# Kernel tuning notes

Measured on AMD Instinct MI355X. Metric: run time of the kernel, lower is better.

Reference implementation:

```python
import jax, jax.numpy as jnp
import numpy as np

B, T, D_MODEL = 2, 2048, 2048
NUM_HEADS, NUM_KV_HEADS, HEAD_DIM = 16, 16, 128
NUM_Q_HEADS = 2 * NUM_HEADS  # diff-v2 doubles the query heads


def _rope_freqs(seqlen, dim_half, base=10000.0):
    inv = 1.0 / (base ** (np.arange(0, dim_half, dtype=np.float32) / dim_half))
    t = np.arange(seqlen, dtype=np.float32)
    ang = np.outer(t, inv)  # [T, dim_half]
    return jnp.asarray(np.cos(ang)), jnp.asarray(np.sin(ang))


def apply_rotary_interleaved(x, cos, sin):
    # x: [B, T, H, D]; cos/sin: [T, D//2]; pairs are adjacent (interleaved=True)
    x1, x2 = x[..., 0::2], x[..., 1::2]
    c = cos[None, :, None, :]
    s = sin[None, :, None, :]
    o1 = x1 * c - x2 * s
    o2 = x1 * s + x2 * c
    return jnp.stack([o1, o2], axis=-1).reshape(x.shape)


def setup_inputs() -> dict:
    key = jax.random.key(0)
    ks = jax.random.split(key, 6)
    x = jax.random.normal(ks[0], (B, T, D_MODEL), dtype=jnp.float32)
    cos, sin = _rope_freqs(T, HEAD_DIM // 2)
    sc = 1.0 / np.sqrt(D_MODEL)
    Wq = jax.random.normal(ks[1], (D_MODEL, NUM_Q_HEADS * HEAD_DIM), dtype=jnp.float32) * sc
    Wk = jax.random.normal(ks[2], (D_MODEL, NUM_KV_HEADS * HEAD_DIM), dtype=jnp.float32) * sc
    Wv = jax.random.normal(ks[3], (D_MODEL, NUM_KV_HEADS * HEAD_DIM), dtype=jnp.float32) * sc
    Wo = jax.random.normal(ks[4], (NUM_HEADS * HEAD_DIM, D_MODEL), dtype=jnp.float32) * sc
    Wlam = jax.random.normal(ks[5], (D_MODEL, NUM_HEADS), dtype=jnp.float32) * sc
    return {"x": x, "cos": cos, "sin": sin, "Wq": Wq, "Wk": Wk, "Wv": Wv, "Wo": Wo, "Wlam": Wlam}


def reference(x, cos, sin, Wq, Wk, Wv, Wo, Wlam):
    b, t, _ = x.shape
    q = (x @ Wq).reshape(b, t, NUM_Q_HEADS, HEAD_DIM)
    k = (x @ Wk).reshape(b, t, NUM_KV_HEADS, HEAD_DIM)
    v = (x @ Wv).reshape(b, t, NUM_KV_HEADS, HEAD_DIM)
    q = apply_rotary_interleaved(q, cos, sin)
    k = apply_rotary_interleaved(k, cos, sin)
    # GQA: repeat kv heads to match the doubled query heads
    rep = NUM_Q_HEADS // NUM_KV_HEADS
    k = jnp.repeat(k, rep, axis=2)
    v = jnp.repeat(v, rep, axis=2)
    scale = 1.0 / np.sqrt(HEAD_DIM)
    scores = jnp.einsum('bthd,bshd->bhts', q, k) * scale  # [B, 2H, T, T]
    causal = jnp.tril(jnp.ones((t, t), dtype=bool))
    scores = jnp.where(causal[None, None], scores, jnp.finfo(scores.dtype).min)
    p = jax.nn.softmax(scores, axis=-1)
    attn = jnp.einsum('bhts,bshd->bthd', p, v)  # [B, T, 2H, D]
    lam = jax.nn.sigmoid(x @ Wlam)  # [B, T, H]
    attn1, attn2 = attn[:, :, 0::2], attn[:, :, 1::2]
    out = attn1 - lam[..., None] * attn2  # [B, T, H, D]
    return out.reshape(b, t, NUM_HEADS * HEAD_DIM) @ Wo
```

## Files before the change

### kernel.cpp

```cpp
#include <hip/hip_runtime.h>

#define T_SEQ 2048
#define BATCH 2
#define DMODEL 2048
#define NQH 32
#define NKVH 16
#define HD 128

typedef _Float16 f16;
typedef _Float16 f16x8 __attribute__((ext_vector_type(8)));
typedef _Float16 f16x4 __attribute__((ext_vector_type(4)));
typedef _Float16 f16x2 __attribute__((ext_vector_type(2)));
typedef float f32x4 __attribute__((ext_vector_type(4)));

typedef const __attribute__((address_space(1))) void* gptr_t;
typedef __attribute__((address_space(3))) void* sptr_t;
#define GLDS16(g, l) __builtin_amdgcn_global_load_lds((gptr_t)(g), (sptr_t)(l), 16, 0, 0)

__global__ __launch_bounds__(256) void k_transpose_all(const float* __restrict__ Wq,
                                                       const float* __restrict__ Wk,
                                                       const float* __restrict__ Wv,
                                                       const float* __restrict__ Wo,
                                                       f16* __restrict__ WqkvT,
                                                       f16* __restrict__ WoT) {
  __shared__ float tile[32][33];
  const int z = blockIdx.z;
  const float* W;
  f16* WT;
  int N;
  if (z == 0)      { W = Wq; WT = WqkvT;                          N = 4096; }
  else if (z == 1) { W = Wk; WT = WqkvT + (size_t)4096 * 2048;    N = 2048; }
  else if (z == 2) { W = Wv; WT = WqkvT + (size_t)6144 * 2048;    N = 2048; }
  else             { W = Wo; WT = WoT;                            N = 2048; }
  const int K = 2048;
  int n0 = blockIdx.x * 32;
  if (n0 >= N) return;
  int k0 = blockIdx.y * 32;
  int tx = threadIdx.x & 31;
  int ty0 = threadIdx.x >> 5;
  #pragma unroll
  for (int i = 0; i < 4; ++i) {
    int ty = ty0 + i * 8;
    tile[ty][tx] = W[(size_t)(k0 + ty) * N + n0 + tx];
  }
  __syncthreads();
  #pragma unroll
  for (int i = 0; i < 4; ++i) {
    int ty = ty0 + i * 8;
    WT[(size_t)(n0 + ty) * K + k0 + tx] = (f16)tile[tx][ty];
  }
}

template<int BM, int BN, int WM, int WN, int OM>
__global__ __launch_bounds__(512, 1) void k_gemm3(const f16* __restrict__ A,
                                                  const f16* __restrict__ BT,
                                                  void* __restrict__ C0,
                                                  f16* __restrict__ Kh,
                                                  f16* __restrict__ VTg,
                                                  const float* __restrict__ cosb,
                                                  const float* __restrict__ sinb,
                                                  int M, int N, int K) {
  constexpr int MR = BM / WM / 16;
  constexpr int MR2 = MR / 2;
  constexpr int NR = BN / WN / 16;
  constexpr int ACH = BM / 64;
  constexpr int BCH = BN / 64;
  __shared__ alignas(16) f16 Al[2][BM * 64];
  __shared__ alignas(16) f16 Bl[2][BN * 64];
  const int tid = threadIdx.x;
  const int lane = tid & 63;
  const int w = tid >> 6;
  const int wr = w / WN, wc = w % WN;
  const int lr = lane & 15, lg = lane >> 4;
  const int nbx = N / BN;
  const int cpx = gridDim.x >> 3;
  const int wg = (blockIdx.x & 7) * cpx + (blockIdx.x >> 3);
  const int m0 = (wg / nbx) * BM, n0 = (wg % nbx) * BN;

#define STAGE_A(BUF, KK)                                                        \
  { _Pragma("unroll")                                                           \
    for (int q = 0; q < ACH; ++q) {                                             \
      int idx = q * 512 + tid; int r = idx >> 3, g = idx & 7;                   \
      GLDS16(A + (size_t)(m0 + r) * K + (KK) + ((g ^ (r & 7)) * 8),             \
             &Al[BUF][idx * 8]);                                                \
    } }
#define STAGE_B(BUF, KK)                                                        \
  { _Pragma("unroll")                                                           \
    for (int q = 0; q < BCH; ++q) {                                             \
      int idx = q * 512 + tid; int r = idx >> 3, g = idx & 7;                   \
      GLDS16(BT + (size_t)(n0 + r) * K + (KK) + ((g ^ (r & 7)) * 8),            \
             &Bl[BUF][idx * 8]);                                                \
    } }
#define LDA8(AF, MH, KH)                                                        \
  { _Pragma("unroll")                                                           \
    for (int i = 0; i < MR2; ++i) {                                             \
      int r = wr * (BM / WM) + ((MH) * MR2 + i) * 16 + lr;                      \
      AF[i] = *(const f16x8*)&Al[buf][r * 64 + ((((KH) * 4 + lg) ^ (r & 7)) * 8)]; \
    } }
#define LDB8(BF, KH)                                                            \
  { _Pragma("unroll")                                                           \
    for (int j = 0; j < NR; ++j) {                                              \
      int r = wc * (BN / WN) + j * 16 + lr;                                     \
      BF[j] = *(const f16x8*)&Bl[buf][r * 64 + ((((KH) * 4 + lg) ^ (r & 7)) * 8)]; \
    } }
#define FMA8(AF, BF, MH)                                                        \
  { __builtin_amdgcn_s_setprio(1);                                              \
    _Pragma("unroll")                                                           \
    for (int i = 0; i < MR2; ++i)                                               \
      _Pragma("unroll")                                                         \
      for (int j = 0; j < NR; ++j)                                              \
        acc[(MH) * MR2 + i][j] =                                                \
          __builtin_amdgcn_mfma_f32_16x16x32_f16(AF[i], BF[j], acc[(MH) * MR2 + i][j], 0, 0, 0); \
    __builtin_amdgcn_s_setprio(0); }
#define PHASE_BAR()                                                             \
  { __builtin_amdgcn_sched_barrier(0); __builtin_amdgcn_s_barrier();            \
    __builtin_amdgcn_sched_barrier(0); }

  f32x4 acc[MR][NR] = {};
  STAGE_A(0, 0);
  STAGE_B(0, 0);
  asm volatile("s_waitcnt vmcnt(0)" ::: "memory");
  __builtin_amdgcn_s_barrier();
  __builtin_amdgcn_sched_barrier(0);

  const int nt = K / 64;
  #pragma unroll 2
  for (int t = 0; t < nt; ++t) {
    const int buf = t & 1;
    f16x8 af[MR2], bf[NR];
    if (t + 1 < nt) STAGE_A(buf ^ 1, (t + 1) * 64);
    LDB8(bf, 0);
    LDA8(af, 0, 0);
    FMA8(af, bf, 0);
    PHASE_BAR();
    if (t + 1 < nt) STAGE_B(buf ^ 1, (t + 1) * 64);
    LDA8(af, 1, 0);
    FMA8(af, bf, 1);
    PHASE_BAR();
    LDB8(bf, 1);
    LDA8(af, 0, 1);
    FMA8(af, bf, 0);
    PHASE_BAR();
    LDA8(af, 1, 1);
    FMA8(af, bf, 1);
    __builtin_amdgcn_sched_barrier(0);
    asm volatile("s_waitcnt vmcnt(0)" ::: "memory");
    __builtin_amdgcn_s_barrier();
    __builtin_amdgcn_sched_barrier(0);
  }
#undef STAGE_A
#undef STAGE_B
#undef LDA8
#undef LDB8
#undef FMA8
#undef PHASE_BAR

  const int mb = m0 + wr * (BM / WM);
  const int nb = n0 + wc * (BN / WN);
  if constexpr (OM == 0) {
    float* C = (float*)C0;
    #pragma unroll
    for (int i = 0; i < MR; ++i)
      #pragma unroll
      for (int j = 0; j < NR; ++j) {
        int r0 = mb + i * 16 + lg * 4;
        int c = nb + j * 16 + lr;
        #pragma unroll
        for (int r = 0; r < 4; ++r)
          C[(size_t)(r0 + r) * N + c] = acc[i][j][r];
      }
  } else {
    if (n0 < 6144) {
      f16* dst = (n0 < 4096) ? (f16*)C0 : Kh;
      const int ncols = (n0 < 4096) ? 4096 : 2048;
      const int coff = (n0 < 4096) ? 0 : 4096;
      #pragma unroll
      for (int i = 0; i < MR; ++i)
        #pragma unroll
        for (int j = 0; j < NR; ++j) {
          int c = nb + j * 16 + lr - coff;
          int jp = (c & 127) >> 1;
          bool odd = (c & 1);
          #pragma unroll
          for (int r = 0; r < 4; ++r) {
            int row = mb + i * 16 + lg * 4 + r;
            int t = row & (T_SEQ - 1);
            float v = acc[i][j][r];
            float pv = __shfl_xor(v, 1);
            float cs = cosb[t * 64 + jp], sn = sinb[t * 64 + jp];
            float out = odd ? (pv * sn + v * cs) : (v * cs - pv * sn);
            dst[(size_t)row * ncols + c] = (f16)out;
          }
        }
    } else {
      #pragma unroll
      for (int i = 0; i < MR; ++i)
        #pragma unroll
        for (int j = 0; j < NR; ++j) {
          int c = nb + j * 16 + lr - 6144;
          int head = c >> 7, d = c & 127;
          int row0 = mb + i * 16 + lg * 4;
          int bb = row0 >> 11, t0 = row0 & (T_SEQ - 1);
          f16x4 zv;
          #pragma unroll
          for (int r = 0; r < 4; ++r) zv[r] = (f16)acc[i][j][r];
          *(f16x4*)(VTg + ((size_t)(bb * NKVH + head) * HD + d) * T_SEQ + t0) = zv;
        }
    }
  }
}

__global__ __launch_bounds__(256) void k_lambda_conv(const float* __restrict__ x,
                                                     const float* __restrict__ Wlam,
                                                     float* __restrict__ lam,
                                                     f16* __restrict__ xh) {
  int row = blockIdx.x;
  const float* xr = x + (size_t)row * DMODEL;
  const int e = threadIdx.x * 8;
  const float4* xp = (const float4*)(xr + e);
  float4 a = xp[0], b2 = xp[1];
  float xv[8] = {a.x, a.y, a.z, a.w, b2.x, b2.y, b2.z, b2.w};
  f16x8 hv;
  #pragma unroll
  for (int j = 0; j < 8; ++j) hv[j] = (f16)xv[j];
  *(f16x8*)(xh + (size_t)row * DMODEL + e) = hv;
  float acc[16];
  #pragma unroll
  for (int h = 0; h < 16; ++h) acc[h] = 0.f;
  #pragma unroll
  for (int j = 0; j < 8; ++j) {
    const float4* wp = (const float4*)(Wlam + (size_t)(e + j) * 16);
    #pragma unroll
    for (int g = 0; g < 4; ++g) {
      float4 wv = wp[g];
      acc[g * 4 + 0] += xv[j] * wv.x; acc[g * 4 + 1] += xv[j] * wv.y;
      acc[g * 4 + 2] += xv[j] * wv.z; acc[g * 4 + 3] += xv[j] * wv.w;
    }
  }
  #pragma unroll
  for (int h = 0; h < 16; ++h)
    for (int off = 32; off > 0; off >>= 1)
      acc[h] += __shfl_down(acc[h], off);
  __shared__ float part[4][16];
  int lane = threadIdx.x & 63, w = threadIdx.x >> 6;
  if (lane == 0) {
    #pragma unroll
    for (int h = 0; h < 16; ++h) part[w][h] = acc[h];
  }
  __syncthreads();
  if (threadIdx.x < 16) {
    float s = part[0][threadIdx.x] + part[1][threadIdx.x] + part[2][threadIdx.x] + part[3][threadIdx.x];
    lam[row * 16 + threadIdx.x] = 1.f / (1.f + __expf(-s));
  }
}

__global__ __launch_bounds__(256, 4) void k_attn4(const f16* __restrict__ Q,
                                                  const f16* __restrict__ K,
                                                  const f16* __restrict__ VT,
                                                  f16* __restrict__ O) {
  __shared__ f16 Kl[64 * 128];
  __shared__ f16 Vl[128 * 64];
  __shared__ f16 Pl[4][16][40];
  const int tid = threadIdx.x;
  const int lane = tid & 63;
  const int w = tid >> 6;
  const int lr = lane & 15, lg = lane >> 4;
  const int flat = blockIdx.x;
  const int xcd = flat & 7;
  const int work = xcd * 128 + (flat >> 3);
  const int grp = work >> 5;
  const int within = work & 31;
  const int b = grp >> 4, hkv = grp & 15;
  const int h = hkv * 2 + (within >> 4);
  const int bx = within & 15;
  const f16* Kg  = K  + (size_t)b * T_SEQ * (NKVH * HD) + hkv * HD;
  const f16* VTg = VT + (size_t)(b * NKVH + hkv) * HD * T_SEQ;
  const float sc = 0.08838834764831845f;

  #pragma unroll 1
  for (int half = 0; half < 2; ++half) {
    const int qt = half ? (31 - bx) : bx;
    const int qb = qt * 64;
    const int qw = qb + w * 16;
    const int qrow = qw + lr;
    f16x8 qf[4];
    {
      const f16* qp = Q + (size_t)(b * T_SEQ + qrow) * (NQH * HD) + h * HD + lg * 8;
      #pragma unroll
      for (int c = 0; c < 4; ++c) qf[c] = *(const f16x8*)(qp + c * 32);
    }
    f32x4 o[8] = {};
    float mi = -1e30f, li = 0.f;

    const int nt = qt + 1;
    #pragma unroll 1
    for (int t = 0; t < nt; ++t) {
      const int s0 = t * 64;
      #pragma unroll
      for (int qq = 0; qq < 4; ++qq) {
        int idx = qq * 256 + tid;
        int r = idx >> 4, g = idx & 15;
        GLDS16(Kg + (size_t)(s0 + r) * (NKVH * HD) + (g ^ (r & 7)) * 8, &Kl[idx * 8]);
      }
      #pragma unroll
      for (int qq = 0; qq < 4; ++qq) {
        int idx = qq * 256 + tid;
        int d = idx >> 3, g = idx & 7;
        GLDS16(VTg + (size_t)d * T_SEQ + s0 + (g ^ (d & 7)) * 8, &Vl[idx * 8]);
      }
      __syncthreads();

      f32x4 sf[4] = {};
      __builtin_amdgcn_s_setprio(1);
      #pragma unroll
      for (int c = 0; c < 4; ++c) {
        #pragma unroll
        for (int nb = 0; nb < 4; ++nb) {
          f16x8 kf = *(const f16x8*)&Kl[(((nb * 16 + lr) * 16) + ((c * 4 + lg) ^ (lr & 7))) * 8];
          sf[nb] = __builtin_amdgcn_mfma_f32_16x16x32_f16(kf, qf[c], sf[nb], 0, 0, 0);
        }
      }
      __builtin_amdgcn_s_setprio(0);
      float v[16];
      #pragma unroll
      for (int nb = 0; nb < 4; ++nb)
        #pragma unroll
        for (int rr = 0; rr < 4; ++rr) {
          float x = sf[nb][rr] * sc;
          int kv = s0 + nb * 16 + lg * 4 + rr;
          v[nb * 4 + rr] = (kv > qrow) ? -1e30f : x;
        }
      float pm = v[0];
      #pragma unroll
      for (int i = 1; i < 16; ++i) pm = fmaxf(pm, v[i]);
      pm = fmaxf(pm, __shfl_xor(pm, 16));
      pm = fmaxf(pm, __shfl_xor(pm, 32));
      float mnew = fmaxf(mi, pm);
      float a = __expf(mi - mnew);
      mi = mnew;
      float rs = 0.f;
      #pragma unroll
      for (int i = 0; i < 16; ++i) { float p = __expf(v[i] - mnew); v[i] = p; rs += p; }
      rs += __shfl_xor(rs, 16);
      rs += __shfl_xor(rs, 32);
      li = a * li + rs;
      float ab[4];
      #pragma unroll
      for (int rr = 0; rr < 4; ++rr) ab[rr] = __shfl(a, lg * 4 + rr);
      #pragma unroll
      for (int j = 0; j < 8; ++j)
        #pragma unroll
        for (int rr = 0; rr < 4; ++rr) o[j][rr] *= ab[rr];
      #pragma unroll
      for (int ks = 0; ks < 2; ++ks) {
        #pragma unroll
        for (int nb2 = 0; nb2 < 2; ++nb2) {
          int nb = ks * 2 + nb2;
          f16x4 pk;
          #pragma unroll
          for (int rr = 0; rr < 4; ++rr) pk[rr] = (f16)v[nb * 4 + rr];
          *(f16x4*)&Pl[w][lr][nb2 * 16 + lg * 4] = pk;
        }
        f16x8 pa = *(const f16x8*)&Pl[w][lr][lg * 8];
        __builtin_amdgcn_s_setprio(1);
        #pragma unroll
        for (int j = 0; j < 8; ++j) {
          f16x8 vbj = *(const f16x8*)&Vl[(((j * 16 + lr) * 8) + ((ks * 4 + lg) ^ (lr & 7))) * 8];
          o[j] = __builtin_amdgcn_mfma_f32_16x16x32_f16(pa, vbj, o[j], 0, 0, 0);
        }
        __builtin_amdgcn_s_setprio(0);
      }
      __syncthreads();
    }
    float lib[4];
    #pragma unroll
    for (int rr = 0; rr < 4; ++rr) lib[rr] = 1.f / __shfl(li, lg * 4 + rr);
    #pragma unroll
    for (int j = 0; j < 8; ++j)
      #pragma unroll
      for (int rr = 0; rr < 4; ++rr) {
        float vv = o[j][rr] * lib[rr];
        O[(size_t)(b * T_SEQ + qw + lg * 4 + rr) * (NQH * HD) + h * HD + j * 16 + lr] = (f16)vv;
      }
  }
}

__global__ void k_combine(const f16* __restrict__ attn, const float* __restrict__ lam,
                          f16* __restrict__ Z) {
  int idx = blockIdx.x * blockDim.x + threadIdx.x;
  int d4 = idx & 31;
  int tmp = idx >> 5;
  int h = tmp & 15;
  int row = tmp >> 4;
  if (row >= BATCH * T_SEQ) return;
  float lv = lam[row * 16 + h];
  f16x4 a1 = *(const f16x4*)(attn + (size_t)row * 4096 + (2 * h) * 128 + d4 * 4);
  f16x4 a2 = *(const f16x4*)(attn + (size_t)row * 4096 + (2 * h + 1) * 128 + d4 * 4);
  f16x4 z;
  #pragma unroll
  for (int e = 0; e < 4; ++e) z[e] = (f16)((float)a1[e] - lv * (float)a2[e]);
  *(f16x4*)(Z + (size_t)row * 2048 + h * 128 + d4 * 4) = z;
}

extern "C" void kernel_launch(void* const* d_in, const int* in_sizes, int n_in,
                              void* d_out, int out_size, void* d_ws, size_t ws_size,
                              hipStream_t stream) {
  const float* x    = (const float*)d_in[0];
  const float* cosb = (const float*)d_in[1];
  const float* sinb = (const float*)d_in[2];
  const float* Wq   = (const float*)d_in[3];
  const float* Wk   = (const float*)d_in[4];
  const float* Wv   = (const float*)d_in[5];
  const float* Wo   = (const float*)d_in[6];
  const float* Wlam = (const float*)d_in[7];

  char* ws = (char*)d_ws;
  f16*  xh     = (f16*)(ws);
  f16*  WqkvT  = (f16*)(ws + 16777216);
  f16*  WoT    = (f16*)(ws + 50331648);
  f16*  Qh     = (f16*)(ws + 58720256);
  f16*  Kh     = (f16*)(ws + 92274688);
  f16*  VTg    = (f16*)(ws + 109051904);
  f16*  At     = (f16*)(ws + 125829120);
  f16*  Zh     = (f16*)(ws + 159383552);
  float* lam   = (float*)(ws + 176160768);

  k_transpose_all<<<dim3(128, 64, 4), 256, 0, stream>>>(Wq, Wk, Wv, Wo, WqkvT, WoT);
  k_lambda_conv<<<4096, 256, 0, stream>>>(x, Wlam, lam, xh);

  k_gemm3<256, 256, 2, 4, 3><<<512, 512, 0, stream>>>(xh, WqkvT, Qh, Kh, VTg,
                                                      cosb, sinb, 4096, 8192, 2048);

  k_attn4<<<1024, 256, 0, stream>>>(Qh, Kh, VTg, At);

  k_combine<<<(BATCH * T_SEQ * 16 * 32) / 256, 256, 0, stream>>>(At, lam, Zh);

  k_gemm3<256, 128, 4, 2, 0><<<256, 512, 0, stream>>>(Zh, WoT, d_out, nullptr, nullptr,
                                                      nullptr, nullptr, 4096, 2048, 2048);
}
```

Before: 495.3 us.

## Split GEMM global-to-LDS staging into quarters interleaved with MFMA phases

Restructures the GEMM main loop so the next K-tile's A and B loads are issued in four smaller chunks, one per compute phase. Partial vmcnt waits and explicit lgkmcnt waits with barriers replace the single full drain at the end of each iteration. The goal is to spread memory traffic across the loop and hide load latency behind MFMA work. It also raises the launch bound to two blocks per CU and changes the output GEMM's warp layout from 4x2 to 2x4, which shifts register pressure and the tile shape each warp computes. The partial wait counts depend on the exact number of issued loads, so any mismatch would create a race.

```diff
diff --git a/kernel.cpp b/kernel.cpp
--- a/kernel.cpp
+++ b/kernel.cpp
@@ -52,7 +52,7 @@
 }
 
 template<int BM, int BN, int WM, int WN, int OM>
-__global__ __launch_bounds__(512, 1) void k_gemm3(const f16* __restrict__ A,
+__global__ __launch_bounds__(512, 2) void k_gemm4(const f16* __restrict__ A,
                                                   const f16* __restrict__ BT,
                                                   void* __restrict__ C0,
                                                   f16* __restrict__ Kh,
@@ -65,6 +65,9 @@
   constexpr int NR = BN / WN / 16;
   constexpr int ACH = BM / 64;
   constexpr int BCH = BN / 64;
+  constexpr int AH = ACH / 2;
+  constexpr int BH = BCH / 2;
+  static_assert(ACH == 4, "A staging split assumes BM==256");
   __shared__ alignas(16) f16 Al[2][BM * 64];
   __shared__ alignas(16) f16 Bl[2][BN * 64];
   const int tid = threadIdx.x;
@@ -77,33 +80,34 @@
   const int wg = (blockIdx.x & 7) * cpx + (blockIdx.x >> 3);
   const int m0 = (wg / nbx) * BM, n0 = (wg % nbx) * BN;
 
-#define STAGE_A(BUF, KK)                                                        \
+#define ST_B(HALF, BB, KK)                                                      \
   { _Pragma("unroll")                                                           \
-    for (int q = 0; q < ACH; ++q) {                                             \
+    for (int q = (HALF) * BH; q < (HALF) * BH + BH; ++q) {                      \
+      int idx = q * 512 + tid; int r = idx >> 3, g = idx & 7;                   \
+      GLDS16(BT + (size_t)(n0 + r) * K + (KK) + ((g ^ (r & 7)) * 8),            \
+             &Bl[BB][idx * 8]);                                                 \
+    } }
+#define ST_A(PAR, BB, KK)                                                       \
+  { _Pragma("unroll")                                                           \
+    for (int i2 = 0; i2 < AH; ++i2) {                                           \
+      int q = 2 * i2 + (PAR);                                                   \
       int idx = q * 512 + tid; int r = idx >> 3, g = idx & 7;                   \
       GLDS16(A + (size_t)(m0 + r) * K + (KK) + ((g ^ (r & 7)) * 8),             \
-             &Al[BUF][idx * 8]);                                                \
+             &Al[BB][idx * 8]);                                                 \
     } }
-#define STAGE_B(BUF, KK)                                                        \
-  { _Pragma("unroll")                                                           \
-    for (int q = 0; q < BCH; ++q) {                                             \
-      int idx = q * 512 + tid; int r = idx >> 3, g = idx & 7;                   \
-      GLDS16(BT + (size_t)(n0 + r) * K + (KK) + ((g ^ (r & 7)) * 8),            \
-             &Bl[BUF][idx * 8]);                                                \
-    } }
-#define LDA8(AF, MH, KH)                                                        \
+#define LDA8(AF, BUF, MH, KH)                                                   \
   { _Pragma("unroll")                                                           \
     for (int i = 0; i < MR2; ++i) {                                             \
       int r = wr * (BM / WM) + ((MH) * MR2 + i) * 16 + lr;                      \
-      AF[i] = *(const f16x8*)&Al[buf][r * 64 + ((((KH) * 4 + lg) ^ (r & 7)) * 8)]; \
+      AF[i] = *(const f16x8*)&Al[BUF][r * 64 + ((((KH) * 4 + lg) ^ (r & 7)) * 8)]; \
     } }
-#define LDB8(BF, KH)                                                            \
+#define LDB8(BF, BUF, KH)                                                       \
   { _Pragma("unroll")                                                           \
     for (int j = 0; j < NR; ++j) {                                              \
       int r = wc * (BN / WN) + j * 16 + lr;                                     \
-      BF[j] = *(const f16x8*)&Bl[buf][r * 64 + ((((KH) * 4 + lg) ^ (r & 7)) * 8)]; \
+      BF[j] = *(const f16x8*)&Bl[BUF][r * 64 + ((((KH) * 4 + lg) ^ (r & 7)) * 8)]; \
     } }
-#define FMA8(AF, BF, MH)                                                        \
+#define FMA16(AF, BF, MH)                                                       \
   { __builtin_amdgcn_s_setprio(1);                                              \
     _Pragma("unroll")                                                           \
     for (int i = 0; i < MR2; ++i)                                               \
@@ -112,48 +116,64 @@
         acc[(MH) * MR2 + i][j] =                                                \
           __builtin_amdgcn_mfma_f32_16x16x32_f16(AF[i], BF[j], acc[(MH) * MR2 + i][j], 0, 0, 0); \
     __builtin_amdgcn_s_setprio(0); }
-#define PHASE_BAR()                                                             \
-  { __builtin_amdgcn_sched_barrier(0); __builtin_amdgcn_s_barrier();            \
-    __builtin_amdgcn_sched_barrier(0); }
+#define BAR() __builtin_amdgcn_s_barrier()
+#define LGKM0() { asm volatile("s_waitcnt lgkmcnt(0)" ::: "memory");            \
+                  __builtin_amdgcn_sched_barrier(0); }
+#define VMW(N) asm volatile("s_waitcnt vmcnt(" #N ")" ::: "memory")
+#define VM_BH() { if constexpr (BH == 2) VMW(2); else VMW(1); }
+#define VM_AH() { VMW(2); }
 
   f32x4 acc[MR][NR] = {};
-  STAGE_A(0, 0);
-  STAGE_B(0, 0);
-  asm volatile("s_waitcnt vmcnt(0)" ::: "memory");
-  __builtin_amdgcn_s_barrier();
-  __builtin_amdgcn_sched_barrier(0);
+  ST_B(0, 0, 0); ST_B(1, 0, 0); ST_A(0, 0, 0); ST_A(1, 0, 0);
+  VM_AH();
+  BAR();
 
   const int nt = K / 64;
   #pragma unroll 2
   for (int t = 0; t < nt; ++t) {
     const int buf = t & 1;
+    const int kk1 = (t + 1) * 64;
+    const bool nxt = (t + 1 < nt);
     f16x8 af[MR2], bf[NR];
-    if (t + 1 < nt) STAGE_A(buf ^ 1, (t + 1) * 64);
-    LDB8(bf, 0);
-    LDA8(af, 0, 0);
-    FMA8(af, bf, 0);
-    PHASE_BAR();
-    if (t + 1 < nt) STAGE_B(buf ^ 1, (t + 1) * 64);
-    LDA8(af, 1, 0);
-    FMA8(af, bf, 1);
-    PHASE_BAR();
-    LDB8(bf, 1);
-    LDA8(af, 0, 1);
-    FMA8(af, bf, 0);
-    PHASE_BAR();
-    LDA8(af, 1, 1);
-    FMA8(af, bf, 1);
-    __builtin_amdgcn_sched_barrier(0);
-    asm volatile("s_waitcnt vmcnt(0)" ::: "memory");
-    __builtin_amdgcn_s_barrier();
-    __builtin_amdgcn_sched_barrier(0);
-  }
-#undef STAGE_A
-#undef STAGE_B
+    if (nxt) ST_B(0, buf ^ 1, kk1);
+    LDB8(bf, buf, 0);
+    LDA8(af, buf, 0, 0);
+    BAR();
+    LGKM0();
+    FMA16(af, bf, 0);
+    if (nxt) { VM_BH(); } else { VMW(0); }
+    BAR();
+    if (nxt) ST_B(1, buf ^ 1, kk1);
+    LDA8(af, buf, 1, 0);
+    BAR();
+    LGKM0();
+    FMA16(af, bf, 1);
+    BAR();
+    if (nxt) ST_A(0, buf ^ 1, kk1);
+    LDB8(bf, buf, 1);
+    LDA8(af, buf, 0, 1);
+    BAR();
+    LGKM0();
+    FMA16(af, bf, 0);
+    BAR();
+    if (nxt) ST_A(1, buf ^ 1, kk1);
+    LDA8(af, buf, 1, 1);
+    BAR();
+    LGKM0();
+    FMA16(af, bf, 1);
+    if (nxt) { VM_AH(); } else { VMW(0); }
+    BAR();
+  }
+#undef ST_B
+#undef ST_A
 #undef LDA8
 #undef LDB8
-#undef FMA8
-#undef PHASE_BAR
+#undef FMA16
+#undef BAR
+#undef LGKM0
+#undef VMW
+#undef VM_BH
+#undef VM_AH
 
   const int mb = m0 + wr * (BM / WM);
   const int nb = n0 + wc * (BN / WN);
@@ -428,13 +448,13 @@
   k_transpose_all<<<dim3(128, 64, 4), 256, 0, stream>>>(Wq, Wk, Wv, Wo, WqkvT, WoT);
   k_lambda_conv<<<4096, 256, 0, stream>>>(x, Wlam, lam, xh);
 
-  k_gemm3<256, 256, 2, 4, 3><<<512, 512, 0, stream>>>(xh, WqkvT, Qh, Kh, VTg,
+  k_gemm4<256, 256, 2, 4, 3><<<512, 512, 0, stream>>>(xh, WqkvT, Qh, Kh, VTg,
                                                       cosb, sinb, 4096, 8192, 2048);
 
   k_attn4<<<1024, 256, 0, stream>>>(Qh, Kh, VTg, At);
 
   k_combine<<<(BATCH * T_SEQ * 16 * 32) / 256, 256, 0, stream>>>(At, lam, Zh);
 
-  k_gemm3<256, 128, 4, 2, 0><<<256, 512, 0, stream>>>(Zh, WoT, d_out, nullptr, nullptr,
+  k_gemm4<256, 128, 2, 4, 0><<<256, 512, 0, stream>>>(Zh, WoT, d_out, nullptr, nullptr,
                                                       nullptr, nullptr, 4096, 2048, 2048);
 }
```

Result: slower. 572.0 us (+15.5%).
